# Kernel tuning notes

Measured on AMD Instinct MI355X. Metric: run time of the kernel, lower is better.

Reference implementation:

```python
import jax, jax.numpy as jnp
import numpy as np

D_MODEL, D_STATE, D_CONV, EXPAND = 1024, 16, 4, 2
D_INNER = EXPAND * D_MODEL
B, L = 2, 4096
LN_EPS = 1e-5


def setup_inputs() -> dict:
    key = jax.random.key(0)
    ks = jax.random.split(key, 6)
    x = jax.random.normal(ks[0], (B, L, D_MODEL), dtype=jnp.float32)
    ln_gamma = jnp.ones((D_MODEL,), jnp.float32)
    ln_beta = jnp.zeros((D_MODEL,), jnp.float32)
    W_in = jax.random.normal(ks[1], (2 * D_INNER, D_MODEL), jnp.float32) / np.sqrt(D_MODEL).astype(np.float32)
    conv_w = jax.random.normal(ks[2], (D_INNER, 1, D_CONV), jnp.float32) * 0.1
    conv_b = jnp.zeros((D_INNER,), jnp.float32)
    W_out = jax.random.normal(ks[3], (D_MODEL, D_INNER), jnp.float32) / np.sqrt(D_INNER).astype(np.float32)
    A = jnp.eye(D_STATE, dtype=jnp.float32)
    Bm = jax.random.normal(ks[4], (D_STATE, D_INNER), jnp.float32) * 0.01
    Cm = jax.random.normal(ks[5], (D_STATE, D_INNER), jnp.float32) * 0.01
    return dict(x=x, ln_gamma=ln_gamma, ln_beta=ln_beta, W_in=W_in,
                conv_w=conv_w, conv_b=conv_b, W_out=W_out, A=A, Bm=Bm, Cm=Cm)


def _layernorm(x, gamma, beta):
    mu = jnp.mean(x, axis=-1, keepdims=True)
    var = jnp.mean(jnp.square(x - mu), axis=-1, keepdims=True)
    return (x - mu) * jax.lax.rsqrt(var + LN_EPS) * gamma + beta


def _causal_depthwise_conv(xp, conv_w, conv_b):
    # xp: (B, L, D_INNER) -> torch Conv1d(padding=K-1, groups=C) then slice [:L]
    # == left-pad K-1, valid depthwise conv.
    lhs = jnp.pad(xp.transpose(0, 2, 1), ((0, 0), (0, 0), (D_CONV - 1, 0)))  # (B,C,L+K-1)
    out = jax.lax.conv_general_dilated(
        lhs, conv_w, window_strides=(1,), padding='VALID',
        dimension_numbers=('NCH', 'OIH', 'NCH'), feature_group_count=D_INNER)
    return out.transpose(0, 2, 1) + conv_b  # (B, L, C)


def reference(x, ln_gamma, ln_beta, W_in, conv_w, conv_b, W_out, A, Bm, Cm):
    # scan permutation is identity (untrained optimizer state); masking disabled
    xn = _layernorm(x, ln_gamma, ln_beta)
    xz = jnp.einsum('bld,ed->ble', xn, W_in)          # (B, L, 2*D_INNER)
    x_part, z = jnp.split(xz, 2, axis=-1)             # each (B, L, D_INNER)
    x_conv = jax.nn.silu(_causal_depthwise_conv(x_part, conv_w, conv_b))

    # recurrence: s_t = s_{t-1} @ A.T + u_t @ B.T ; out_t = (x_conv_t + s_t @ C) * sigmoid(z_t)
    u_seq = x_part.transpose(1, 0, 2)                 # (L, B, D_INNER)
    xc_seq = x_conv.transpose(1, 0, 2)
    z_seq = z.transpose(1, 0, 2)

    def step(state, inp):
        u_t, xc_t, z_t = inp
        state = state @ A.T + u_t @ Bm.T              # (B, D_STATE)
        out = (xc_t + state @ Cm) * jax.nn.sigmoid(z_t)
        return state, out

    state0 = jnp.zeros((x.shape[0], D_STATE), x.dtype)
    _, ys = jax.lax.scan(step, state0, (u_seq, xc_seq, z_seq))
    y = ys.transpose(1, 0, 2)                         # (B, L, D_INNER)
    residual = jnp.einsum('bli,di->bld', y, W_out)    # (B, L, D_MODEL)
    return x + residual
```

## Files before the change

### kernel.cpp

```cpp
#include <hip/hip_runtime.h>
#include <hip/hip_bf16.h>
#include <math.h>

#define D_MODEL 1024
#define D_STATE 16
#define D_CONV 4
#define D_INNER 2048
#define BATCH 2
#define SEQ 4096
#define NROW (BATCH * SEQ)
#define LN_EPS 1e-5f

typedef __attribute__((ext_vector_type(8))) short  bf16x8_t;
typedef __attribute__((ext_vector_type(4))) float  f32x4_t;
typedef __attribute__((ext_vector_type(8))) unsigned short u16x8_t;

__device__ inline unsigned short f2bf(float f) {
    unsigned u = __float_as_uint(f);
    u += 0x7fffu + ((u >> 16) & 1u);
    return (unsigned short)(u >> 16);
}
__device__ inline float bf2f(unsigned short u) {
    return __uint_as_float((unsigned)u << 16);
}

#define GLL16(g, l)                                                            \
    __builtin_amdgcn_global_load_lds(                                          \
        (const __attribute__((address_space(1))) void*)(g),                    \
        (__attribute__((address_space(3))) void*)(l), 16, 0, 0)

#define FENCE asm volatile("" ::: "memory")
#define BAR do { FENCE; __builtin_amdgcn_s_barrier(); FENCE; } while (0)

#define CVT_BLOCKS 3088
__global__ __launch_bounds__(256) void pre_kernel(const float* __restrict__ x,
                                                  const float* __restrict__ gamma,
                                                  const float* __restrict__ beta,
                                                  const float* __restrict__ W_in,
                                                  const float* __restrict__ W_out,
                                                  const float* __restrict__ Bm,
                                                  unsigned short* __restrict__ xn,
                                                  unsigned short* __restrict__ Win_bf,
                                                  unsigned short* __restrict__ Wout_bf,
                                                  unsigned short* __restrict__ Bm_bf) {
    __shared__ float red[8];
    const int tid = threadIdx.x;
    if (blockIdx.x < CVT_BLOCKS) {
        const long long g = (long long)(blockIdx.x * 256 + tid) * 8;
        const long long n1 = (long long)2 * D_INNER * D_MODEL;
        const long long n2 = n1 + (long long)D_MODEL * D_INNER;
        const float* src; unsigned short* dst; long long off;
        if (g < n1)      { src = W_in;  dst = Win_bf;  off = g; }
        else if (g < n2) { src = W_out; dst = Wout_bf; off = g - n1; }
        else             { src = Bm;    dst = Bm_bf;   off = g - n2; }
        const float4 a = *reinterpret_cast<const float4*>(src + off);
        const float4 b = *reinterpret_cast<const float4*>(src + off + 4);
        u16x8_t p;
        p[0] = f2bf(a.x); p[1] = f2bf(a.y); p[2] = f2bf(a.z); p[3] = f2bf(a.w);
        p[4] = f2bf(b.x); p[5] = f2bf(b.y); p[6] = f2bf(b.z); p[7] = f2bf(b.w);
        *reinterpret_cast<u16x8_t*>(dst + off) = p;
        return;
    }
    const int row = blockIdx.x - CVT_BLOCKS;
    const float4* xr = reinterpret_cast<const float4*>(x + (size_t)row * D_MODEL);
    float4 v = xr[tid];

    const int lane = tid & 63, wave = tid >> 6;
    float s = v.x + v.y + v.z + v.w;
    #pragma unroll
    for (int off = 32; off > 0; off >>= 1) s += __shfl_down(s, off, 64);
    if (lane == 0) red[wave] = s;
    __syncthreads();
    float mu = (red[0] + red[1] + red[2] + red[3]) * (1.0f / D_MODEL);
    __syncthreads();

    float dx = v.x - mu, dy = v.y - mu, dz = v.z - mu, dw = v.w - mu;
    float ss = dx * dx + dy * dy + dz * dz + dw * dw;
    #pragma unroll
    for (int off = 32; off > 0; off >>= 1) ss += __shfl_down(ss, off, 64);
    if (lane == 0) red[wave] = ss;
    __syncthreads();
    float var = (red[0] + red[1] + red[2] + red[3]) * (1.0f / D_MODEL);
    float rs = rsqrtf(var + LN_EPS);

    const float4 gv = reinterpret_cast<const float4*>(gamma)[tid];
    const float4 bv = reinterpret_cast<const float4*>(beta)[tid];
    ushort4 o;
    o.x = f2bf(dx * rs * gv.x + bv.x);
    o.y = f2bf(dy * rs * gv.y + bv.y);
    o.z = f2bf(dz * rs * gv.z + bv.z);
    o.w = f2bf(dw * rs * gv.w + bv.w);
    reinterpret_cast<ushort4*>(xn + (size_t)row * D_MODEL)[tid] = o;
}

__global__ __launch_bounds__(512) void gemm256_bf16(const short* __restrict__ A,
                                                    const short* __restrict__ B,
                                                    unsigned short* __restrict__ Cb,
                                                    int M, int N, int K) {
    __shared__ short lds[2 * 4 * 8192];

    const int tid = threadIdx.x;
    const int w = tid >> 6, l = tid & 63;
    const int row0 = blockIdx.y * 256;
    const int col0 = blockIdx.x * 256;
    const int wm = w >> 2;
    const int wn = w & 3;
    const int fr = l & 15;
    const int fc = (l >> 4) * 8;
    const int NT = K >> 6;

    const int qa = wm;
    const int qb = 2 + (wn >> 1);
    const int bb = (wn & 1) * 64;

    auto STAGE = [&](const short* __restrict__ G, int growbase, int k0,
                     int buf, int q) {
        #pragma unroll
        for (int j = 0; j < 2; ++j) {
            const int e = ((j * 8 + w) << 9) + l * 8;
            const int r = e >> 6;
            const int c = (e & 63) ^ ((r & 7) << 3);
            GLL16(G + (size_t)(growbase + r) * K + k0 + c,
                  &lds[buf * 32768 + q * 8192 + ((j * 8 + w) << 9)]);
        }
    };
    auto LDF = [&](int buf, int q, int r, int ks) -> bf16x8_t {
        const int c = (ks * 32 + fc) ^ ((r & 7) << 3);
        return *reinterpret_cast<const bf16x8_t*>(
            &lds[buf * 32768 + q * 8192 + r * 64 + c]);
    };

    f32x4_t acc[8][4] = {};
    bf16x8_t af[4][2], bA[2][2], bB[2][2];

#define MFMA_Q(mh, nh, bfr)                                                    \
    do {                                                                       \
        _Pragma("unroll")                                                      \
        for (int mi = 0; mi < 4; ++mi)                                         \
            _Pragma("unroll")                                                  \
            for (int ni = 0; ni < 2; ++ni)                                     \
                _Pragma("unroll")                                              \
                for (int ks = 0; ks < 2; ++ks)                                 \
                    acc[(mh) * 4 + mi][(nh) * 2 + ni] =                        \
                        __builtin_amdgcn_mfma_f32_16x16x32_bf16(               \
                            af[mi][ks], bfr[ni][ks],                           \
                            acc[(mh) * 4 + mi][(nh) * 2 + ni], 0, 0, 0);       \
    } while (0)

    STAGE(A, row0,       0, 0, 0);
    STAGE(A, row0 + 128, 0, 0, 1);
    STAGE(B, col0,       0, 0, 2);
    STAGE(B, col0 + 128, 0, 0, 3);
    if (NT > 1) {
        STAGE(B, col0,       64, 1, 2);
        STAGE(B, col0 + 128, 64, 1, 3);
        STAGE(A, row0,       64, 1, 0);
        asm volatile("s_waitcnt vmcnt(6)" ::: "memory");
    } else {
        asm volatile("s_waitcnt vmcnt(0)" ::: "memory");
    }
    BAR;

    for (int kt = 0; kt < NT; ++kt) {
        const int buf = kt & 1, nbuf = buf ^ 1;
        #pragma unroll
        for (int mi = 0; mi < 4; ++mi)
            #pragma unroll
            for (int ks = 0; ks < 2; ++ks)
                af[mi][ks] = LDF(buf, qa, mi * 16 + fr, ks);
        #pragma unroll
        for (int ni = 0; ni < 2; ++ni)
            #pragma unroll
            for (int ks = 0; ks < 2; ++ks)
                bA[ni][ks] = LDF(buf, qb, bb + ni * 16 + fr, ks);
        if (kt + 1 < NT) STAGE(A, row0 + 128, (kt + 1) << 6, nbuf, 1);
        BAR;
        __builtin_amdgcn_s_setprio(1);
        MFMA_Q(0, 0, bA);
        __builtin_amdgcn_s_setprio(0);
        BAR;
        #pragma unroll
        for (int ni = 0; ni < 2; ++ni)
            #pragma unroll
            for (int ks = 0; ks < 2; ++ks)
                bB[ni][ks] = LDF(buf, qb, bb + 32 + ni * 16 + fr, ks);
        BAR;
        __builtin_amdgcn_s_setprio(1);
        MFMA_Q(0, 1, bB);
        __builtin_amdgcn_s_setprio(0);
        BAR;
        #pragma unroll
        for (int mi = 0; mi < 4; ++mi)
            #pragma unroll
            for (int ks = 0; ks < 2; ++ks)
                af[mi][ks] = LDF(buf, qa, 64 + mi * 16 + fr, ks);
        if (kt + 2 < NT) {
            STAGE(B, col0,       (kt + 2) << 6, buf, 2);
            STAGE(B, col0 + 128, (kt + 2) << 6, buf, 3);
        }
        BAR;
        __builtin_amdgcn_s_setprio(1);
        MFMA_Q(1, 1, bB);
        __builtin_amdgcn_s_setprio(0);
        BAR;
        if (kt + 2 < NT) {
            STAGE(A, row0, (kt + 2) << 6, buf, 0);
            asm volatile("s_waitcnt vmcnt(6)" ::: "memory");
        } else {
            asm volatile("s_waitcnt vmcnt(0)" ::: "memory");
        }
        BAR;
        __builtin_amdgcn_s_setprio(1);
        MFMA_Q(1, 0, bA);
        __builtin_amdgcn_s_setprio(0);
        BAR;
    }
#undef MFMA_Q

    const int cr = (l >> 4) * 4;
    const int cc = l & 15;
    #pragma unroll
    for (int m = 0; m < 8; ++m) {
        #pragma unroll
        for (int n = 0; n < 4; ++n) {
            size_t base = (size_t)(row0 + wm * 128 + m * 16 + cr) * N +
                          (col0 + wn * 64 + n * 16 + cc);
            #pragma unroll
            for (int j = 0; j < 4; ++j)
                Cb[base + (size_t)j * N] = f2bf(acc[m][n][j]);
        }
    }
}

__global__ __launch_bounds__(512) void gemm_out(const short* __restrict__ A,
                                                const short* __restrict__ B,
                                                const float* __restrict__ add,
                                                float* __restrict__ C,
                                                int M, int N, int K) {
    __shared__ short lds[3 * 3 * 8192];

    const int tid = threadIdx.x;
    const int w = tid >> 6, l = tid & 63;

    const int id = blockIdx.y * gridDim.x + blockIdx.x;
    const int cpx = (gridDim.x * gridDim.y) >> 3;
    const int sid = (id & 7) * cpx + (id >> 3);
    const int row0 = (sid / gridDim.x) * 256;
    const int col0 = (sid % gridDim.x) * 128;

    const int wm = w >> 2;
    const int wn = w & 3;
    const int fr = l & 15;
    const int fc = (l >> 4) * 8;
    const int NT = K >> 6;
    const int bb = wn * 32;

    auto STAGE = [&](const short* __restrict__ G, int growbase, int k0,
                     int buf, int q) {
        #pragma unroll
        for (int j = 0; j < 2; ++j) {
            const int e = ((j * 8 + w) << 9) + l * 8;
            const int r = e >> 6;
            const int c = (e & 63) ^ ((r & 7) << 3);
            GLL16(G + (size_t)(growbase + r) * K + k0 + c,
                  &lds[buf * 24576 + q * 8192 + ((j * 8 + w) << 9)]);
        }
    };
    auto LDF = [&](int buf, int q, int r, int ks) -> bf16x8_t {
        const int c = (ks * 32 + fc) ^ ((r & 7) << 3);
        return *reinterpret_cast<const bf16x8_t*>(
            &lds[buf * 24576 + q * 8192 + r * 64 + c]);
    };

    f32x4_t acc[8][2] = {};
    bf16x8_t af[4][2], af2[4][2], bA[2], bB[2];

#define MFMA_H(AF, mh, an, BFR)                                                \
    do {                                                                       \
        _Pragma("unroll")                                                      \
        for (int mi = 0; mi < 4; ++mi)                                         \
            _Pragma("unroll")                                                  \
            for (int ks = 0; ks < 2; ++ks)                                     \
                acc[(mh) * 4 + mi][(an)] =                                     \
                    __builtin_amdgcn_mfma_f32_16x16x32_bf16(                   \
                        AF[mi][ks], BFR[ks], acc[(mh) * 4 + mi][(an)], 0, 0, 0);\
    } while (0)

    STAGE(A, row0,       0, 0, 0);
    STAGE(A, row0 + 128, 0, 0, 1);
    STAGE(B, col0,       0, 0, 2);
    if (NT > 1) {
        STAGE(A, row0,       64, 1, 0);
        STAGE(A, row0 + 128, 64, 1, 1);
        STAGE(B, col0,       64, 1, 2);
        asm volatile("s_waitcnt vmcnt(6)" ::: "memory");
    } else {
        asm volatile("s_waitcnt vmcnt(0)" ::: "memory");
    }

    int buf = 0;
    for (int kt = 0; kt < NT; ++kt) {
        BAR;
        #pragma unroll
        for (int mi = 0; mi < 4; ++mi)
            #pragma unroll
            for (int ks = 0; ks < 2; ++ks) {
                af[mi][ks]  = LDF(buf, wm, mi * 16 + fr, ks);
                af2[mi][ks] = LDF(buf, wm, 64 + mi * 16 + fr, ks);
            }
        #pragma unroll
        for (int ks = 0; ks < 2; ++ks) {
            bA[ks] = LDF(buf, 2, bb + fr, ks);
            bB[ks] = LDF(buf, 2, bb + 16 + fr, ks);
        }
        __builtin_amdgcn_s_setprio(1);
        MFMA_H(af,  0, 0, bA);
        MFMA_H(af2, 1, 0, bA);
        MFMA_H(af,  0, 1, bB);
        MFMA_H(af2, 1, 1, bB);
        __builtin_amdgcn_s_setprio(0);
        if (kt + 2 < NT) {
            const int sb = (buf + 2) % 3;
            STAGE(A, row0,       (kt + 2) << 6, sb, 0);
            STAGE(A, row0 + 128, (kt + 2) << 6, sb, 1);
            STAGE(B, col0,       (kt + 2) << 6, sb, 2);
            asm volatile("s_waitcnt vmcnt(6)" ::: "memory");
        } else {
            asm volatile("s_waitcnt vmcnt(0)" ::: "memory");
        }
        buf = (buf + 1) % 3;
    }
#undef MFMA_H

    const int cr = (l >> 4) * 4;
    const int cc = l & 15;
    #pragma unroll
    for (int m = 0; m < 8; ++m) {
        #pragma unroll
        for (int n = 0; n < 2; ++n) {
            size_t base = (size_t)(row0 + wm * 128 + m * 16 + cr) * N +
                          (col0 + wn * 32 + n * 16 + cc);
            #pragma unroll
            for (int j = 0; j < 4; ++j)
                C[base + (size_t)j * N] = acc[m][n][j] + add[base + (size_t)j * N];
        }
    }
}

__global__ __launch_bounds__(64) void v_mfma(const unsigned short* __restrict__ xz,
                                             const unsigned short* __restrict__ Bmb,
                                             float* __restrict__ V) {
    const int l = threadIdx.x;
    const int r0 = blockIdx.x * 16;
    const int fr = l & 15;
    const int fk = (l >> 4) * 8;

    const unsigned short* aP = xz + (size_t)(r0 + fr) * (2 * D_INNER) + fk;
    const unsigned short* bP = Bmb + fr * D_INNER + fk;

    f32x4_t acc = {};
    #pragma unroll 4
    for (int k0 = 0; k0 < D_INNER; k0 += 32) {
        bf16x8_t a = *reinterpret_cast<const bf16x8_t*>(aP + k0);
        bf16x8_t b = *reinterpret_cast<const bf16x8_t*>(bP + k0);
        acc = __builtin_amdgcn_mfma_f32_16x16x32_bf16(a, b, acc, 0, 0, 0);
    }

    const int cr = (l >> 4) * 4;
    const int cc = l & 15;
    #pragma unroll
    for (int j = 0; j < 4; ++j)
        V[(size_t)(r0 + cr + j) * D_STATE + cc] = acc[j];
}

__global__ __launch_bounds__(256) void scan_par(const float* __restrict__ V,
                                                const float* __restrict__ A,
                                                float* __restrict__ S) {
    __shared__ int nid;
    const int tid = threadIdx.x;
    if (tid == 0) nid = 0;
    __syncthreads();
    {
        const float ex = ((tid >> 4) == (tid & 15)) ? 1.0f : 0.0f;
        if (A[tid] != ex) atomicOr(&nid, 1);
    }
    __syncthreads();
    if (nid) return;

    const int p = blockIdx.x;
    const int b = p >> 4, s = p & 15;
    const float* vb = V + (size_t)b * SEQ * D_STATE + s;
    float* sb = S + (size_t)b * SEQ * D_STATE + s;

    const int t0 = tid * 16;
    float v[16];
    float run = 0.0f;
    #pragma unroll
    for (int j = 0; j < 16; ++j) {
        run += vb[(size_t)(t0 + j) * D_STATE];
        v[j] = run;
    }

    const float tot = run;
    float sc = tot;
    #pragma unroll
    for (int off = 1; off < 64; off <<= 1) {
        float n = __shfl_up(sc, off, 64);
        if ((tid & 63) >= off) sc += n;
    }
    __shared__ float wtot[4];
    if ((tid & 63) == 63) wtot[tid >> 6] = sc;
    __syncthreads();
    float woff = 0.0f;
    #pragma unroll
    for (int w2 = 0; w2 < 4; ++w2)
        if (w2 < (tid >> 6)) woff += wtot[w2];
    const float excl = sc - tot + woff;

    #pragma unroll
    for (int j = 0; j < 16; ++j)
        sb[(size_t)(t0 + j) * D_STATE] = v[j] + excl;
}

#define SCAN_CHUNK 256

__global__ __launch_bounds__(64) void scan_seq(const float* __restrict__ V,
                                               const float* __restrict__ A,
                                               float* __restrict__ S) {
    const int tid = threadIdx.x;
    int bad = 0;
    for (int i = tid; i < D_STATE * D_STATE; i += 64) {
        const float ex = ((i >> 4) == (i & 15)) ? 1.0f : 0.0f;
        if (A[i] != ex) bad = 1;
    }
    if (__ballot(bad) == 0ULL) return;

    __shared__ float Al[D_STATE * D_STATE];
    __shared__ float Vl[2 * SCAN_CHUNK * D_STATE];
    __shared__ float Sl[2 * SCAN_CHUNK * D_STATE];

    for (int i = tid; i < D_STATE * D_STATE; i += 64) Al[i] = A[i];
    __syncthreads();

    float st = 0.0f;
    const int bb = (tid >> 4) & 1;
    const int ss = tid & 15;

    for (int t0 = 0; t0 < SEQ; t0 += SCAN_CHUNK) {
        for (int idx = tid; idx < 2 * SCAN_CHUNK * D_STATE; idx += 64) {
            int b = idx >> 12;
            int rem = idx & 4095;
            Vl[idx] = V[((size_t)(b * SEQ + t0) * D_STATE) + rem];
        }
        __syncthreads();

        if (tid < 32) {
            float* vb = Vl + bb * SCAN_CHUNK * D_STATE + ss;
            float* sb = Sl + bb * SCAN_CHUNK * D_STATE + ss;
            for (int t = 0; t < SCAN_CHUNK; ++t) {
                float ns = vb[t * D_STATE];
                #pragma unroll
                for (int s2 = 0; s2 < D_STATE; ++s2) {
                    float other = __shfl(st, (tid & 16) | s2, 64);
                    ns = fmaf(Al[ss * D_STATE + s2], other, ns);
                }
                st = ns;
                sb[t * D_STATE] = st;
            }
        }
        __syncthreads();

        for (int idx = tid; idx < 2 * SCAN_CHUNK * D_STATE; idx += 64) {
            int b = idx >> 12;
            int rem = idx & 4095;
            S[((size_t)(b * SEQ + t0) * D_STATE) + rem] = Sl[idx];
        }
        __syncthreads();
    }
}

__global__ __launch_bounds__(256) void y_kernel(const unsigned short* __restrict__ xz,
                                                const float* __restrict__ S,
                                                const float* __restrict__ Cm,
                                                const float* __restrict__ convw,
                                                const float* __restrict__ convb,
                                                unsigned short* __restrict__ y) {
    const int tid = threadIdx.x;
    const int i0 = blockIdx.x * 512 + tid * 2;
    const int r0 = blockIdx.y * 64;
    const int tb0 = r0 & (SEQ - 1);

    const float4 w0 = *reinterpret_cast<const float4*>(&convw[i0 * D_CONV]);
    const float4 w1 = *reinterpret_cast<const float4*>(&convw[(i0 + 1) * D_CONV]);
    const float cb0 = convb[i0], cb1 = convb[i0 + 1];
    float cm0[D_STATE], cm1[D_STATE];
    #pragma unroll
    for (int s = 0; s < D_STATE; ++s) {
        float2 c = *reinterpret_cast<const float2*>(&Cm[s * D_INNER + i0]);
        cm0[s] = c.x; cm1[s] = c.y;
    }

    float2 xm1 = make_float2(0.f, 0.f), xm2 = xm1, xm3 = xm1;
    if (tb0 >= 1) { ushort2 u = *reinterpret_cast<const ushort2*>(&xz[(size_t)(r0 - 1) * (2 * D_INNER) + i0]); xm1 = make_float2(bf2f(u.x), bf2f(u.y)); }
    if (tb0 >= 2) { ushort2 u = *reinterpret_cast<const ushort2*>(&xz[(size_t)(r0 - 2) * (2 * D_INNER) + i0]); xm2 = make_float2(bf2f(u.x), bf2f(u.y)); }
    if (tb0 >= 3) { ushort2 u = *reinterpret_cast<const ushort2*>(&xz[(size_t)(r0 - 3) * (2 * D_INNER) + i0]); xm3 = make_float2(bf2f(u.x), bf2f(u.y)); }

    for (int r = r0; r < r0 + 64; ++r) {
        const ushort2 xu = *reinterpret_cast<const ushort2*>(&xz[(size_t)r * (2 * D_INNER) + i0]);
        const ushort2 zu = *reinterpret_cast<const ushort2*>(&xz[(size_t)r * (2 * D_INNER) + D_INNER + i0]);
        const float2 x0 = make_float2(bf2f(xu.x), bf2f(xu.y));

        float a0 = cb0;
        a0 = fmaf(w0.x, xm3.x, a0); a0 = fmaf(w0.y, xm2.x, a0);
        a0 = fmaf(w0.z, xm1.x, a0); a0 = fmaf(w0.w, x0.x, a0);
        float a1 = cb1;
        a1 = fmaf(w1.x, xm3.y, a1); a1 = fmaf(w1.y, xm2.y, a1);
        a1 = fmaf(w1.z, xm1.y, a1); a1 = fmaf(w1.w, x0.y, a1);

        const float xc0 = a0 / (1.0f + expf(-a0));
        const float xc1 = a1 / (1.0f + expf(-a1));

        const float4* Sp = reinterpret_cast<const float4*>(S + (size_t)r * D_STATE);
        const float4 s0 = Sp[0], s1 = Sp[1], s2 = Sp[2], s3 = Sp[3];
        const float sv[D_STATE] = {s0.x, s0.y, s0.z, s0.w, s1.x, s1.y, s1.z, s1.w,
                                   s2.x, s2.y, s2.z, s2.w, s3.x, s3.y, s3.z, s3.w};
        float sc0 = 0.f, sc1 = 0.f;
        #pragma unroll
        for (int s = 0; s < D_STATE; ++s) {
            sc0 = fmaf(sv[s], cm0[s], sc0);
            sc1 = fmaf(sv[s], cm1[s], sc1);
        }

        const float z0 = bf2f(zu.x), z1 = bf2f(zu.y);
        const float g0 = 1.0f / (1.0f + expf(-z0));
        const float g1 = 1.0f / (1.0f + expf(-z1));

        ushort2 o;
        o.x = f2bf((xc0 + sc0) * g0);
        o.y = f2bf((xc1 + sc1) * g1);
        *reinterpret_cast<ushort2*>(&y[(size_t)r * D_INNER + i0]) = o;

        xm3 = xm2; xm2 = xm1; xm1 = x0;
    }
}

extern "C" void kernel_launch(void* const* d_in, const int* in_sizes, int n_in,
                              void* d_out, int out_size, void* d_ws, size_t ws_size,
                              hipStream_t stream) {
    const float* x      = (const float*)d_in[0];
    const float* ln_g   = (const float*)d_in[1];
    const float* ln_b   = (const float*)d_in[2];
    const float* W_in   = (const float*)d_in[3];
    const float* conv_w = (const float*)d_in[4];
    const float* conv_b = (const float*)d_in[5];
    const float* W_out  = (const float*)d_in[6];
    const float* A      = (const float*)d_in[7];
    const float* Bm     = (const float*)d_in[8];
    const float* Cm     = (const float*)d_in[9];
    float* out = (float*)d_out;

    float* ws = (float*)d_ws;
    float* V  = ws;
    float* S  = V + (size_t)NROW * D_STATE;
    unsigned short* xz_bf  = (unsigned short*)(S + (size_t)NROW * D_STATE);
    unsigned short* xn_bf  = xz_bf  + (size_t)NROW * 2 * D_INNER;
    unsigned short* Win_bf = xn_bf  + (size_t)NROW * D_MODEL;
    unsigned short* Wout_bf= Win_bf + (size_t)(2 * D_INNER) * D_MODEL;
    unsigned short* Bm_bf  = Wout_bf + (size_t)D_MODEL * D_INNER;
    unsigned short* y_bf   = Bm_bf  + (size_t)D_STATE * D_INNER;

    pre_kernel<<<CVT_BLOCKS + NROW, 256, 0, stream>>>(
        x, ln_g, ln_b, W_in, W_out, Bm, xn_bf, Win_bf, Wout_bf, Bm_bf);

    gemm256_bf16<<<dim3((2 * D_INNER) / 256, NROW / 256), 512, 0, stream>>>(
        (const short*)xn_bf, (const short*)Win_bf, xz_bf,
        NROW, 2 * D_INNER, D_MODEL);

    v_mfma<<<NROW / 16, 64, 0, stream>>>(xz_bf, Bm_bf, V);

    scan_par<<<32, 256, 0, stream>>>(V, A, S);
    scan_seq<<<1, 64, 0, stream>>>(V, A, S);

    y_kernel<<<dim3(D_INNER / 512, NROW / 64), 256, 0, stream>>>(
        xz_bf, S, Cm, conv_w, conv_b, y_bf);

    gemm_out<<<dim3(D_MODEL / 128, NROW / 256), 512, 0, stream>>>(
        (const short*)y_bf, (const short*)Wout_bf, x, out,
        NROW, D_MODEL, D_INNER);
}
```

Measured before the change: 196.1 us.

## Batch LDS fragment loads per k-tile, cut barriers, remap blocks across XCDs

Each k-tile iteration of the bf16 GEMM now loads all A and B fragments into registers up front, issues the global prefetches, and then runs all four MFMA quadrants back to back. This drops the old four-phase barrier ping-pong, so there are far fewer workgroup barriers per tile. Block IDs are remapped so consecutive tiles land on the same XCD chunk for better L2 reuse, and launch bounds now request 2 blocks per CU. The extra af2 register set raises VGPR pressure and gives up the fine-grained overlap between LDS reads and MFMAs. With 512 threads, 2 blocks per CU may also force spills.

```diff
diff --git a/kernel.cpp b/kernel.cpp
--- a/kernel.cpp
+++ b/kernel.cpp
@@ -93,16 +93,21 @@
     reinterpret_cast<ushort4*>(xn + (size_t)row * D_MODEL)[tid] = o;
 }
 
-__global__ __launch_bounds__(512) void gemm256_bf16(const short* __restrict__ A,
-                                                    const short* __restrict__ B,
-                                                    unsigned short* __restrict__ Cb,
-                                                    int M, int N, int K) {
+__global__ __launch_bounds__(512, 2) void gemm256_bf16(const short* __restrict__ A,
+                                                       const short* __restrict__ B,
+                                                       unsigned short* __restrict__ Cb,
+                                                       int M, int N, int K) {
     __shared__ short lds[2 * 4 * 8192];
 
     const int tid = threadIdx.x;
     const int w = tid >> 6, l = tid & 63;
-    const int row0 = blockIdx.y * 256;
-    const int col0 = blockIdx.x * 256;
+
+    const int id = blockIdx.y * gridDim.x + blockIdx.x;
+    const int cpx = (gridDim.x * gridDim.y) >> 3;
+    const int sid = (id & 7) * cpx + (id >> 3);
+    const int row0 = (sid / gridDim.x) * 256;
+    const int col0 = (sid % gridDim.x) * 256;
+
     const int wm = w >> 2;
     const int wn = w & 3;
     const int fr = l & 15;
@@ -131,9 +136,9 @@
     };
 
     f32x4_t acc[8][4] = {};
-    bf16x8_t af[4][2], bA[2][2], bB[2][2];
-
-#define MFMA_Q(mh, nh, bfr)                                                    \
+    bf16x8_t af[4][2], af2[4][2], bA[2][2], bB[2][2];
+
+#define MFMA_Q(AF, mh, nh, BFR)                                                \
     do {                                                                       \
         _Pragma("unroll")                                                      \
         for (int mi = 0; mi < 4; ++mi)                                         \
@@ -143,7 +148,7 @@
                 for (int ks = 0; ks < 2; ++ks)                                 \
                     acc[(mh) * 4 + mi][(nh) * 2 + ni] =                        \
                         __builtin_amdgcn_mfma_f32_16x16x32_bf16(               \
-                            af[mi][ks], bfr[ni][ks],                           \
+                            AF[mi][ks], BFR[ni][ks],                           \
                             acc[(mh) * 4 + mi][(nh) * 2 + ni], 0, 0, 0);       \
     } while (0)
 
@@ -173,47 +178,34 @@
             #pragma unroll
             for (int ks = 0; ks < 2; ++ks)
                 bA[ni][ks] = LDF(buf, qb, bb + ni * 16 + fr, ks);
-        if (kt + 1 < NT) STAGE(A, row0 + 128, (kt + 1) << 6, nbuf, 1);
-        BAR;
-        __builtin_amdgcn_s_setprio(1);
-        MFMA_Q(0, 0, bA);
-        __builtin_amdgcn_s_setprio(0);
-        BAR;
         #pragma unroll
         for (int ni = 0; ni < 2; ++ni)
             #pragma unroll
             for (int ks = 0; ks < 2; ++ks)
                 bB[ni][ks] = LDF(buf, qb, bb + 32 + ni * 16 + fr, ks);
+        #pragma unroll
+        for (int mi = 0; mi < 4; ++mi)
+            #pragma unroll
+            for (int ks = 0; ks < 2; ++ks)
+                af2[mi][ks] = LDF(buf, qa, 64 + mi * 16 + fr, ks);
+        if (kt + 1 < NT) STAGE(A, row0 + 128, (kt + 1) << 6, nbuf, 1);
+        asm volatile("s_waitcnt lgkmcnt(0)" ::: "memory");
         BAR;
-        __builtin_amdgcn_s_setprio(1);
-        MFMA_Q(0, 1, bB);
-        __builtin_amdgcn_s_setprio(0);
-        BAR;
-        #pragma unroll
-        for (int mi = 0; mi < 4; ++mi)
-            #pragma unroll
-            for (int ks = 0; ks < 2; ++ks)
-                af[mi][ks] = LDF(buf, qa, 64 + mi * 16 + fr, ks);
         if (kt + 2 < NT) {
             STAGE(B, col0,       (kt + 2) << 6, buf, 2);
             STAGE(B, col0 + 128, (kt + 2) << 6, buf, 3);
-        }
-        BAR;
-        __builtin_amdgcn_s_setprio(1);
-        MFMA_Q(1, 1, bB);
-        __builtin_amdgcn_s_setprio(0);
-        BAR;
-        if (kt + 2 < NT) {
-            STAGE(A, row0, (kt + 2) << 6, buf, 0);
+            STAGE(A, row0,       (kt + 2) << 6, buf, 0);
             asm volatile("s_waitcnt vmcnt(6)" ::: "memory");
         } else {
             asm volatile("s_waitcnt vmcnt(0)" ::: "memory");
         }
         BAR;
         __builtin_amdgcn_s_setprio(1);
-        MFMA_Q(1, 0, bA);
+        MFMA_Q(af,  0, 0, bA);
+        MFMA_Q(af,  0, 1, bB);
+        MFMA_Q(af2, 1, 1, bB);
+        MFMA_Q(af2, 1, 0, bA);
         __builtin_amdgcn_s_setprio(0);
-        BAR;
     }
 #undef MFMA_Q
 
```

Measured after the change: 193.6 us. About the same (-1.3%).
